# Performance work log

Measured on AMD Instinct MI355X. Metric: run time of the kernel, lower is better.

Reference implementation:

```python
import jax, jax.numpy as jnp
import numpy as np
from jax import lax

BN_EPS = 1e-3
SLOPE = 0.1
CLUSTER_TEMP = 30.0
K = 16
FEAT = 4096  # 8*8*64


def conv_bn_lrelu(x, w, b, g, beta, m, v):
    # Conv2d stride 2, padding 1 (NCHW / OIHW), then eval-mode BatchNorm, then LeakyReLU.
    y = lax.conv_general_dilated(x, w, window_strides=(2, 2), padding=((1, 1), (1, 1)),
                                 dimension_numbers=("NCHW", "OIHW", "NCHW"))
    y = y + b[None, :, None, None]
    scale = g / jnp.sqrt(v + BN_EPS)
    y = y * scale[None, :, None, None] + (beta - m * scale)[None, :, None, None]
    return jnp.where(y > 0, y, SLOPE * y)


def soft_kmeans(data, mu, num_iter, ct):
    # Row L2-normalize (equivalent to diag(1/||x||) @ data)
    data = data / jnp.linalg.norm(data, axis=1, keepdims=True)
    for _ in range(num_iter):
        dist = data @ mu.T                      # [N, K]
        r = jax.nn.softmax(ct * dist, axis=1)   # [N, K]
        mu = (r.T @ data) / r.sum(axis=0)[:, None]  # [K, F]
    dist = data @ mu.T
    r = jax.nn.softmax(ct * dist, axis=1)
    return mu, r, dist


def setup_inputs() -> dict:
    key = jax.random.key(0)
    ks = jax.random.split(key, 12)
    d = {}
    d["x"] = jax.random.normal(ks[0], (256, 3, 64, 64), dtype=jnp.float32)
    # conv1: 3 -> 128
    d["conv1_w"] = jax.random.normal(ks[1], (128, 3, 3, 3), dtype=jnp.float32) * 0.05
    d["conv1_b"] = jnp.zeros((128,), jnp.float32)
    d["bn1_g"] = jnp.ones((128,), jnp.float32)
    d["bn1_b"] = jnp.zeros((128,), jnp.float32)
    d["bn1_m"] = jax.random.normal(ks[2], (128,), dtype=jnp.float32) * 0.1
    d["bn1_v"] = jax.random.uniform(ks[3], (128,), minval=0.5, maxval=1.5, dtype=jnp.float32)
    # conv2: 128 -> 256
    d["conv2_w"] = jax.random.normal(ks[4], (256, 128, 3, 3), dtype=jnp.float32) * 0.02
    d["conv2_b"] = jnp.zeros((256,), jnp.float32)
    d["bn2_g"] = jnp.ones((256,), jnp.float32)
    d["bn2_b"] = jnp.zeros((256,), jnp.float32)
    d["bn2_m"] = jax.random.normal(ks[5], (256,), dtype=jnp.float32) * 0.1
    d["bn2_v"] = jax.random.uniform(ks[6], (256,), minval=0.5, maxval=1.5, dtype=jnp.float32)
    # conv3: 256 -> 64
    d["conv3_w"] = jax.random.normal(ks[7], (64, 256, 3, 3), dtype=jnp.float32) * 0.02
    d["conv3_b"] = jnp.zeros((64,), jnp.float32)
    d["bn3_g"] = jnp.ones((64,), jnp.float32)
    d["bn3_b"] = jnp.zeros((64,), jnp.float32)
    d["bn3_m"] = jax.random.normal(ks[8], (64,), dtype=jnp.float32) * 0.1
    d["bn3_v"] = jax.random.uniform(ks[9], (64,), minval=0.5, maxval=1.5, dtype=jnp.float32)
    # initial cluster centers, torch.rand(K, F)
    d["mu0"] = jax.random.uniform(ks[10], (K, FEAT), dtype=jnp.float32)
    d["num_iter"] = 10
    return d


def reference(x, conv1_w, conv1_b, bn1_g, bn1_b, bn1_m, bn1_v,
              conv2_w, conv2_b, bn2_g, bn2_b, bn2_m, bn2_v,
              conv3_w, conv3_b, bn3_g, bn3_b, bn3_m, bn3_v,
              mu0, num_iter):
    h = conv_bn_lrelu(x, conv1_w, conv1_b, bn1_g, bn1_b, bn1_m, bn1_v)   # [B,128,32,32]
    h = conv_bn_lrelu(h, conv2_w, conv2_b, bn2_g, bn2_b, bn2_m, bn2_v)   # [B,256,16,16]
    h = conv_bn_lrelu(h, conv3_w, conv3_b, bn3_g, bn3_b, bn3_m, bn3_v)   # [B,64,8,8]
    embeds = h.reshape(-1, FEAT)                                          # [B, 4096]
    mu_init, _, _ = soft_kmeans(embeds, mu0, num_iter, CLUSTER_TEMP)
    _, r, _ = soft_kmeans(embeds, lax.stop_gradient(mu_init), 1, CLUSTER_TEMP)
    return r
```

## Files before the change

kernel.cpp:

```cpp
#include <hip/hip_runtime.h>
#include <stdint.h>
#include <stddef.h>

typedef unsigned short u16;
typedef __attribute__((ext_vector_type(8))) short short8;
typedef __attribute__((ext_vector_type(4))) float f32x4;
typedef __attribute__((ext_vector_type(4))) int int4v;

__device__ __forceinline__ float bf2f(u16 u) {
    unsigned x = ((unsigned)u) << 16;
    return __uint_as_float(x);
}
__device__ __forceinline__ u16 f2bf(float f) {
    unsigned x = __float_as_uint(f);
    unsigned r = (x + 0x7fffu + ((x >> 16) & 1u)) >> 16;
    return (u16)r;
}
__device__ __forceinline__ float ldin(const void* p, size_t i, int isbf) {
    return isbf ? bf2f(((const u16*)p)[i]) : ((const float*)p)[i];
}
__device__ __forceinline__ int detect_bf(const void* v1) {
    const u16* ub = (const u16*)v1;
    int ok = 1;
#pragma unroll
    for (int i = 0; i < 16; i++) {
        float f = bf2f(ub[i]);
        if (!(f >= 0.4f && f <= 1.6f)) ok = 0;
    }
    return ok;
}
__device__ __forceinline__ int sw(int r, int c8) {
    return r * 32 + (((c8) ^ (r & 3)) << 3);
}

struct PrepArgs {
    const void *w1, *w2, *w3;
    u16 *W1p, *W2p, *W3p;
    const void *b1, *g1, *be1, *m1, *v1;
    const void *b2, *g2, *be2, *m2, *v2;
    const void *b3, *g3, *be3, *m3, *v3;
    float *es1, *esh1, *es2, *esh2, *es3, *esh3;
    u16 *zb;
};
__device__ __forceinline__ void packw_body(const void* src, u16* dst, int CI, int Kp,
                                           int total, int blk, int t, int isbf) {
    int p = blk * 256 + t;
    if (p >= total) return;
    int co = p / Kp, k = p - co * Kp;
    int tap = k / CI, ci = k - tap * CI;
    u16 v = 0;
    if (tap < 9) {
        size_t si = (size_t)(co * CI + ci) * 9 + tap;
        v = isbf ? ((const u16*)src)[si] : f2bf(((const float*)src)[si]);
    }
    dst[p] = v;
}
__global__ __launch_bounds__(256) void kprep_all(PrepArgs A) {
    int b = blockIdx.x, t = threadIdx.x;
    int isbf = detect_bf(A.v1);
    if (b < 1152) {
        packw_body(A.w2, A.W2p, 128, 1152, 256 * 1152, b, t, isbf);
    } else if (b < 1728) {
        packw_body(A.w3, A.W3p, 256, 2304, 64 * 2304, b - 1152, t, isbf);
    } else if (b < 1744) {
        packw_body(A.w1, A.W1p, 3, 32, 128 * 32, b - 1728, t, isbf);
    } else {
        if (b == 1745) A.zb[t] = 0;
        int u = (b - 1744) * 256 + t;
        const void *bb, *g, *be, *m, *v;
        float *es, *esh;
        int c;
        if (u < 128)      { c = u;       bb=A.b1; g=A.g1; be=A.be1; m=A.m1; v=A.v1; es=A.es1; esh=A.esh1; }
        else if (u < 384) { c = u - 128; bb=A.b2; g=A.g2; be=A.be2; m=A.m2; v=A.v2; es=A.es2; esh=A.esh2; }
        else if (u < 448) { c = u - 384; bb=A.b3; g=A.g3; be=A.be3; m=A.m3; v=A.v3; es=A.es3; esh=A.esh3; }
        else return;
        float sc = ldin(g, c, isbf) / sqrtf(ldin(v, c, isbf) + 1e-3f);
        float sh = (ldin(bb, c, isbf) - ldin(m, c, isbf)) * sc + ldin(be, c, isbf);
        es[c] = sc;
        esh[c] = sh;
    }
}

__global__ void kfallback(u16* __restrict__ out) {
    int i = blockIdx.x * 256 + threadIdx.x;
    if (i < 4096) out[i] = f2bf(0.0625f);
}

__global__ __launch_bounds__(256) void im2col1(const void* __restrict__ x,
                                               u16* __restrict__ A1,
                                               const void* __restrict__ v1ref) {
    int n = blockIdx.x, t = threadIdx.x;
    int isbf = detect_bf(v1ref);
    __shared__ u16 xs[3 * 64 * 64];
    if (isbf) {
        const u16* xp = (const u16*)x + (size_t)n * 12288;
#pragma unroll
        for (int i = t * 8; i < 12288; i += 2048)
            *(int4v*)&xs[i] = *(const int4v*)&xp[i];
    } else {
        const float* xp = (const float*)x + (size_t)n * 12288;
#pragma unroll
        for (int i = t * 4; i < 12288; i += 1024) {
            float4 v = *(const float4*)&xp[i];
            xs[i] = f2bf(v.x); xs[i + 1] = f2bf(v.y);
            xs[i + 2] = f2bf(v.z); xs[i + 3] = f2bf(v.w);
        }
    }
    __syncthreads();
#pragma unroll
    for (int rr = 0; rr < 4; rr++) {
        int m = rr * 256 + t;
        int ox = m & 31, oy = m >> 5;
        alignas(16) u16 row[32];
#pragma unroll
        for (int k = 0; k < 32; k++) {
            u16 val = 0;
            if (k < 27) {
                int tap = k / 3, ci = k - 3 * tap;
                int ky = tap / 3, kx = tap - 3 * ky;
                int iy = 2 * oy - 1 + ky, ix = 2 * ox - 1 + kx;
                if ((unsigned)iy < 64u && (unsigned)ix < 64u)
                    val = xs[ci * 4096 + iy * 64 + ix];
            }
            row[k] = val;
        }
        int4v* dst = (int4v*)(A1 + ((size_t)n * 1024 + m) * 32);
        const int4v* srcv = (const int4v*)row;
#pragma unroll
        for (int q = 0; q < 4; q++) dst[q] = srcv[q];
    }
}

__global__ __launch_bounds__(256) void gemm_conv1(
    const u16* __restrict__ A1, const u16* __restrict__ W,
    const float* __restrict__ es, const float* __restrict__ esh,
    u16* __restrict__ OutB) {
    alignas(16) __shared__ u16 As[128 * 32];
    alignas(16) __shared__ u16 Bs[128 * 32];
    const int t = threadIdx.x;
    const int m0 = blockIdx.x * 128;
    const int lane = t & 63, w = t >> 6;
    const int wm = w & 1, wn = w >> 1;
    const int rA = t >> 2, c8 = t & 3, koff = c8 * 8;

#pragma unroll
    for (int j = 0; j < 2; j++) {
        int4v va = *(const int4v*)(A1 + (size_t)(m0 + j * 64 + rA) * 32 + koff);
        *(int4v*)&As[sw(j * 64 + rA, c8)] = va;
        int4v vb = *(const int4v*)(W + (size_t)(j * 64 + rA) * 32 + koff);
        *(int4v*)&Bs[sw(j * 64 + rA, c8)] = vb;
    }
    __syncthreads();
    const int qc = lane >> 4, fr = lane & 15;
    short8 af[4], bf[4];
#pragma unroll
    for (int i = 0; i < 4; i++) af[i] = *(const short8*)&As[sw(wm * 64 + i * 16 + fr, qc)];
#pragma unroll
    for (int j = 0; j < 4; j++) bf[j] = *(const short8*)&Bs[sw(wn * 64 + j * 16 + fr, qc)];
    f32x4 acc[4][4];
#pragma unroll
    for (int i = 0; i < 4; i++)
#pragma unroll
        for (int j = 0; j < 4; j++) {
#pragma unroll
            for (int q = 0; q < 4; q++) acc[i][j][q] = 0.f;
            acc[i][j] = __builtin_amdgcn_mfma_f32_16x16x32_bf16(af[i], bf[j], acc[i][j], 0, 0, 0);
        }
    float scv[4], shv[4];
#pragma unroll
    for (int j = 0; j < 4; j++) {
        int c = wn * 64 + j * 16 + fr;
        scv[j] = es[c];
        shv[j] = esh[c];
    }
#pragma unroll
    for (int i = 0; i < 4; i++) {
#pragma unroll
        for (int rg = 0; rg < 4; rg++) {
            int m = m0 + wm * 64 + i * 16 + qc * 4 + rg;
            int ox = m & 31, oy = (m >> 5) & 31, n = m >> 10;
            u16* orow = OutB + ((size_t)(n * 32 + oy) * 32 + ox) * 128 + wn * 64 + fr;
#pragma unroll
            for (int j = 0; j < 4; j++) {
                float v = acc[i][j][rg] * scv[j] + shv[j];
                v = (v > 0.f) ? v : 0.1f * v;
                orow[j * 16] = f2bf(v);
            }
        }
    }
}

__global__ __launch_bounds__(512, 2) void gemm_conv2(
    const u16* __restrict__ h1, const u16* __restrict__ W,
    const float* __restrict__ es, const float* __restrict__ esh,
    u16* __restrict__ OutB, const u16* __restrict__ zb) {
    alignas(16) __shared__ u16 smem[4 * 16384];
    u16* const Ab0 = smem;
    u16* const Ab1 = smem + 16384;
    u16* const Bb0 = smem + 32768;
    u16* const Bb1 = smem + 49152;

    const int t = threadIdx.x;
    const int w = t >> 6, l = t & 63;
    const int img = blockIdx.x;
    const int wm = w >> 2, wn = w & 3;
    const int fr = l & 15, qc = l >> 4;

    int aiy0[4], aix0[4], ac8e[4];
    int brow[4];
#pragma unroll
    for (int i = 0; i < 4; ++i) {
        int gi = w * 256 + i * 64 + l;
        int r = gi >> 3, c8d = gi & 7;
        int c8s = c8d ^ (r & 7);
        int oy = r >> 4, ox = r & 15;
        aiy0[i] = 2 * oy - 1;
        aix0[i] = 2 * ox - 1;
        ac8e[i] = c8s * 8;
        brow[i] = r * 1152 + c8s * 8;
    }
    auto mkA = [&](int i, int ky, int kx) -> const u16* {
        int iy = aiy0[i] + ky, ix = aix0[i] + kx;
        if ((unsigned)iy < 32u && (unsigned)ix < 32u)
            return h1 + (size_t)(((img * 32 + iy) * 32 + ix) * 128 + ac8e[i]);
        return zb;
    };
    auto stage = [&](const u16* src, u16* ldsbase, int i) {
        __builtin_amdgcn_global_load_lds(
            (const __attribute__((address_space(1))) void*)src,
            (__attribute__((address_space(3))) void*)(ldsbase + (w * 4 + i) * 512),
            16, 0, 0);
    };

    f32x4 acc[8][4];
#pragma unroll
    for (int mi = 0; mi < 8; ++mi)
#pragma unroll
        for (int nj = 0; nj < 4; ++nj)
#pragma unroll
            for (int q = 0; q < 4; ++q) acc[mi][nj][q] = 0.0f;

    auto do_tile = [&](const u16* A, const u16* B) {
#pragma unroll
        for (int kk = 0; kk < 2; ++kk) {
            const int c8 = kk * 4 + qc;
            short8 a[8], b[4];
#pragma unroll
            for (int q = 0; q < 8; ++q) {
                int row = wm * 128 + q * 16 + fr;
                a[q] = *(const short8*)(A + row * 64 + ((c8 ^ (row & 7)) << 3));
            }
#pragma unroll
            for (int j = 0; j < 4; ++j) {
                int row = wn * 64 + j * 16 + fr;
                b[j] = *(const short8*)(B + row * 64 + ((c8 ^ (row & 7)) << 3));
            }
            __builtin_amdgcn_s_setprio(1);
#pragma unroll
            for (int q = 0; q < 8; ++q)
#pragma unroll
                for (int j = 0; j < 4; ++j)
                    acc[q][j] = __builtin_amdgcn_mfma_f32_16x16x32_bf16(
                        a[q], b[j], acc[q][j], 0, 0, 0);
            __builtin_amdgcn_s_setprio(0);
        }
    };

    const u16* pcur[4];
#pragma unroll
    for (int i = 0; i < 4; ++i) pcur[i] = mkA(i, 0, 0);
#pragma unroll
    for (int i = 0; i < 4; ++i) {
        stage(pcur[i], Ab0, i);
        stage(W + brow[i], Bb0, i);
    }

    for (int tap = 0; tap < 9; ++tap) {
        __syncthreads();
#pragma unroll
        for (int i = 0; i < 4; ++i) {
            stage(pcur[i] + 64, Ab1, i);
            stage(W + brow[i] + (2 * tap + 1) * 64, Bb1, i);
        }
        do_tile(Ab0, Bb0);
        __syncthreads();
        if (tap < 8) {
            const int tap2 = tap + 1;
            const int ky2 = (tap2 >= 6) ? 2 : (tap2 >= 3) ? 1 : 0;
            const int kx2 = tap2 - 3 * ky2;
#pragma unroll
            for (int i = 0; i < 4; ++i) pcur[i] = mkA(i, ky2, kx2);
#pragma unroll
            for (int i = 0; i < 4; ++i) {
                stage(pcur[i], Ab0, i);
                stage(W + brow[i] + (2 * tap + 2) * 64, Bb0, i);
            }
        }
        do_tile(Ab1, Bb1);
    }

    float scv[4], shv[4];
#pragma unroll
    for (int nj = 0; nj < 4; ++nj) {
        int c = wn * 64 + nj * 16 + fr;
        scv[nj] = es[c];
        shv[nj] = esh[c];
    }
#pragma unroll
    for (int mi = 0; mi < 8; ++mi) {
#pragma unroll
        for (int rg = 0; rg < 4; ++rg) {
            int r = wm * 128 + mi * 16 + qc * 4 + rg;
            u16* orow = OutB + ((size_t)img * 256 + r) * 256 + wn * 64 + fr;
#pragma unroll
            for (int nj = 0; nj < 4; ++nj) {
                float v = acc[mi][nj][rg] * scv[nj] + shv[nj];
                v = (v > 0.f) ? v : 0.1f * v;
                orow[nj * 16] = f2bf(v);
            }
        }
    }
}

__global__ __launch_bounds__(256) void gemm_conv3f(
    const u16* __restrict__ Asrc, const u16* __restrict__ W,
    const float* __restrict__ es3, const float* __restrict__ esh3,
    float* __restrict__ dat, u16* __restrict__ datbf) {
    constexpr int CIN = 256, KTOT = 2304, IH = 16;
    constexpr int CC = 8, SM = 2, SN = 2;

    alignas(16) __shared__ u16 As[64 * 32];
    alignas(16) __shared__ u16 Bs[64 * 32];
    __shared__ float red[4];

    const int t = threadIdx.x;
    const int lid = blockIdx.x;
    const int xcd = lid & 7, slot = lid >> 3;
    const int img = xcd * 32 + slot;
    const int m0 = img * 64;
    const int lane = t & 63, w = t >> 6;
    const int wm = w & 1, wn = w >> 1;
    const int rA = t >> 2, c8 = t & 3, koff = c8 * 8;
    const int fr = lane & 15, qc = lane >> 4;

    f32x4 acc[SM][SN];
#pragma unroll
    for (int i = 0; i < SM; i++)
#pragma unroll
        for (int j = 0; j < SN; j++)
#pragma unroll
            for (int q = 0; q < 4; q++) acc[i][j][q] = 0.0f;

    const int aox = rA & 7, aoy = (rA >> 3) & 7;
    auto mkoffs = [&](int tap) -> int {
        int ky = tap / 3, kx = tap - 3 * ky;
        int iy = 2 * aoy - 1 + ky, ix = 2 * aox - 1 + kx;
        if ((unsigned)iy < (unsigned)IH && (unsigned)ix < (unsigned)IH)
            return ((img * IH + iy) * IH + ix) * CIN;
        return -0x40000000;
    };
    const u16* Wrow = W + (size_t)rA * KTOT + koff;

    int offs_cur = mkoffs(0), offs_nxt;
    const int4v zerov = (int4v){0, 0, 0, 0};
    int4v bufA[2], bufB[2];
#pragma unroll
    for (int pp = 0; pp < 2; pp++) {
        bufA[pp] = (offs_cur >= 0)
                       ? *(const int4v*)(Asrc + offs_cur + pp * 32 + koff)
                       : zerov;
        bufB[pp] = *(const int4v*)(Wrow + pp * 32);
    }

    int flat = 0;
    for (int tap = 0; tap < 9; tap++) {
        offs_nxt = (tap < 8) ? mkoffs(tap + 1) : -0x40000000;
#pragma unroll
        for (int cc = 0; cc < CC; cc++, flat++) {
            const int pb_ = flat & 1;
            *(int4v*)&As[sw(rA, c8)] = bufA[pb_];
            *(int4v*)&Bs[sw(rA, c8)] = bufB[pb_];
            __syncthreads();
            {
                const int cc2 = cc + 2;
                const bool intap = (cc2 < CC);
                const int cci = intap ? cc2 : cc2 - CC;
                int o = intap ? offs_cur : offs_nxt;
                bufA[pb_] = (o >= 0) ? *(const int4v*)(Asrc + o + cci * 32 + koff) : zerov;
                const bool wvalid = intap || (tap < 8);
                const int wk = (intap ? tap : tap + 1) * CIN + cci * 32;
                bufB[pb_] = wvalid ? *(const int4v*)(Wrow + wk) : zerov;
            }
            short8 af[SM], bf[SN];
#pragma unroll
            for (int i = 0; i < SM; i++)
                af[i] = *(const short8*)&As[sw(wm * 32 + i * 16 + fr, qc)];
#pragma unroll
            for (int j = 0; j < SN; j++)
                bf[j] = *(const short8*)&Bs[sw(wn * 32 + j * 16 + fr, qc)];
#pragma unroll
            for (int i = 0; i < SM; i++)
#pragma unroll
                for (int j = 0; j < SN; j++)
                    acc[i][j] = __builtin_amdgcn_mfma_f32_16x16x32_bf16(
                        af[i], bf[j], acc[i][j], 0, 0, 0);
            __syncthreads();
        }
        offs_cur = offs_nxt;
    }

    float vals[SM][SN][4];
    float ssq = 0.f;
#pragma unroll
    for (int j = 0; j < SN; j++) {
        int c = wn * 32 + j * 16 + fr;
        float sc = es3[c], sh = esh3[c];
#pragma unroll
        for (int i = 0; i < SM; i++) {
#pragma unroll
            for (int rg = 0; rg < 4; rg++) {
                float v = acc[i][j][rg] * sc + sh;
                v = (v > 0.f) ? v : 0.1f * v;
                vals[i][j][rg] = v;
                ssq += v * v;
            }
        }
    }
#pragma unroll
    for (int off = 32; off > 0; off >>= 1) ssq += __shfl_xor(ssq, off);
    if (lane == 0) red[w] = ssq;
    __syncthreads();
    float inv = 1.0f / sqrtf(red[0] + red[1] + red[2] + red[3]);
#pragma unroll
    for (int j = 0; j < SN; j++) {
        int c = wn * 32 + j * 16 + fr;
#pragma unroll
        for (int i = 0; i < SM; i++) {
#pragma unroll
            for (int rg = 0; rg < 4; rg++) {
                int row = wm * 32 + i * 16 + qc * 4 + rg;
                size_t idx = (size_t)img * 4096 + c * 64 + row;
                float v = vals[i][j][rg] * inv;
                dat[idx] = v;
                datbf[idx] = f2bf(v);
            }
        }
    }
}

__global__ __launch_bounds__(256) void kgr(const u16* __restrict__ dbf,
                                           const float* __restrict__ dat,
                                           const void* __restrict__ mu0,
                                           float* __restrict__ Gp,
                                           float* __restrict__ rb0,
                                           const void* __restrict__ v1ref) {
    const int b = blockIdx.x, t = threadIdx.x;
    __shared__ float part[16][4];
    __shared__ float ds[16];

    if (b < 64) {
        const int tile = b & 15, s = b >> 4;
        const int m0 = (tile & 3) * 64, n0 = (tile >> 2) * 64;
        const int lane = t & 63, w = t >> 6;
        const int wm = w & 1, wn = w >> 1;
        const int fr = lane & 15, qc = lane >> 4;

        f32x4 acc[2][2];
#pragma unroll
        for (int i = 0; i < 2; i++)
#pragma unroll
            for (int j = 0; j < 2; j++)
#pragma unroll
                for (int q = 0; q < 4; q++) acc[i][j][q] = 0.0f;

        const u16* a0p = dbf + (size_t)(m0 + wm * 32 + fr) * 4096 + s * 1024 + qc * 8;
        const u16* a1p = a0p + 16 * 4096;
        const u16* b0p = dbf + (size_t)(n0 + wn * 32 + fr) * 4096 + s * 1024 + qc * 8;
        const u16* b1p = b0p + 16 * 4096;

        short8 Pa0[4], Pa1[4], Pb0[4], Pb1[4];
        short8 Qa0[4], Qa1[4], Qb0[4], Qb1[4];
        auto ldc = [&](short8* A0, short8* A1, short8* B0, short8* B1, int c) {
#pragma unroll
            for (int u = 0; u < 4; ++u) {
                const int o = c * 128 + u * 32;
                A0[u] = *(const short8*)(a0p + o);
                A1[u] = *(const short8*)(a1p + o);
                B0[u] = *(const short8*)(b0p + o);
                B1[u] = *(const short8*)(b1p + o);
            }
        };
        auto mmc = [&](short8* A0, short8* A1, short8* B0, short8* B1) {
#pragma unroll
            for (int u = 0; u < 4; ++u) {
                acc[0][0] = __builtin_amdgcn_mfma_f32_16x16x32_bf16(A0[u], B0[u], acc[0][0], 0, 0, 0);
                acc[0][1] = __builtin_amdgcn_mfma_f32_16x16x32_bf16(A0[u], B1[u], acc[0][1], 0, 0, 0);
                acc[1][0] = __builtin_amdgcn_mfma_f32_16x16x32_bf16(A1[u], B0[u], acc[1][0], 0, 0, 0);
                acc[1][1] = __builtin_amdgcn_mfma_f32_16x16x32_bf16(A1[u], B1[u], acc[1][1], 0, 0, 0);
            }
        };
        ldc(Pa0, Pa1, Pb0, Pb1, 0);
#pragma unroll
        for (int c = 0; c < 4; ++c) {
            ldc(Qa0, Qa1, Qb0, Qb1, 2 * c + 1);
            mmc(Pa0, Pa1, Pb0, Pb1);
            if (c < 3) ldc(Pa0, Pa1, Pb0, Pb1, 2 * c + 2);
            mmc(Qa0, Qa1, Qb0, Qb1);
        }

        float* gp = Gp + (size_t)s * 65536;
#pragma unroll
        for (int j = 0; j < 2; j++) {
            int cc = n0 + wn * 32 + j * 16 + fr;
#pragma unroll
            for (int i = 0; i < 2; i++)
#pragma unroll
                for (int rg = 0; rg < 4; rg++) {
                    int row = m0 + wm * 32 + i * 16 + qc * 4 + rg;
                    gp[row * 256 + cc] = acc[i][j][rg];
                }
        }
    } else {
        const int n = b - 64;
        const int isbf = detect_bf(v1ref);
        const int lane = t & 63, wv = t >> 6;
        float d[16];
#pragma unroll
        for (int j = 0; j < 16; j++) d[j] = dat[(size_t)n * 4096 + j * 256 + t];
#pragma unroll
        for (int k = 0; k < 16; k++) {
            float a = 0.f;
            if (isbf) {
                const u16* mp = (const u16*)mu0 + (size_t)k * 4096;
#pragma unroll
                for (int j = 0; j < 16; j++) a = fmaf(d[j], bf2f(mp[j * 256 + t]), a);
            } else {
                const float* mp = (const float*)mu0 + (size_t)k * 4096;
#pragma unroll
                for (int j = 0; j < 16; j++) a = fmaf(d[j], mp[j * 256 + t], a);
            }
#pragma unroll
            for (int off = 32; off > 0; off >>= 1) a += __shfl_xor(a, off);
            if (lane == 0) part[k][wv] = a;
        }
        __syncthreads();
        if (t < 16) {
            float dk = part[t][0] + part[t][1] + part[t][2] + part[t][3];
            ds[t] = dk;
            __syncthreads();
            float mx = -1e30f;
#pragma unroll
            for (int j = 0; j < 16; j++) mx = fmaxf(mx, ds[j]);
            float sum = 0.f;
#pragma unroll
            for (int j = 0; j < 16; j++) sum += __expf(30.f * (ds[j] - mx));
            rb0[n * 16 + t] = __expf(30.f * (dk - mx)) / sum;
        }
    }
}

__global__ __launch_bounds__(256) void kcomb(const float* __restrict__ Gp,
                                             u16* __restrict__ Ghi,
                                             u16* __restrict__ Glo) {
    const int i = (blockIdx.x * 256 + threadIdx.x) * 4;
    f32x4 s0 = *(const f32x4*)(Gp + i);
    f32x4 s1 = *(const f32x4*)(Gp + 65536 + i);
    f32x4 s2 = *(const f32x4*)(Gp + 131072 + i);
    f32x4 s3 = *(const f32x4*)(Gp + 196608 + i);
    unsigned long long ph = 0, pl = 0;
#pragma unroll
    for (int q = 0; q < 4; q++) {
        float v = ((s0[q] + s1[q]) + s2[q]) + s3[q];
        u16 hi = f2bf(v);
        u16 lo = f2bf(v - bf2f(hi));
        ph |= ((unsigned long long)hi) << (16 * q);
        pl |= ((unsigned long long)lo) << (16 * q);
    }
    *(unsigned long long*)(Ghi + i) = ph;
    *(unsigned long long*)(Glo + i) = pl;
}

__global__ __launch_bounds__(1024) void kmiter(const u16* __restrict__ Ghi,
                                               const u16* __restrict__ Glo,
                                               const float* __restrict__ rb0,
                                               void* __restrict__ dout,
                                               const void* __restrict__ v1ref) {
    const int t = threadIdx.x;
    const int isbf = detect_bf(v1ref);
    const int lane = t & 63, w = t >> 6;
    const int i0 = w * 16;
    const int col = lane & 15;
    const int q = lane >> 4;

    __shared__ u16 rThi[16 * 264];
    __shared__ u16 rTlo[16 * 264];
    __shared__ float part[16][17];

    const u16* Ahirow = Ghi + (size_t)(i0 + col) * 256 + q * 8;
    const u16* Alorow = Glo + (size_t)(i0 + col) * 256 + q * 8;

    {
        float rv[4];
#pragma unroll
        for (int rg = 0; rg < 4; rg++) {
            int row = i0 + q * 4 + rg;
            float v = rb0[row * 16 + col];
            rv[rg] = v;
            u16 hi = f2bf(v);
            rThi[col * 264 + row] = hi;
            rTlo[col * 264 + row] = f2bf(v - bf2f(hi));
        }
        float s0 = rv[0] + rv[1] + rv[2] + rv[3];
        s0 += __shfl_xor(s0, 16);
        s0 += __shfl_xor(s0, 32);
        if (lane < 16) part[w][lane] = s0;
    }
    __syncthreads();
    float rsc = 0.f;
#pragma unroll
    for (int ww = 0; ww < 16; ww++) rsc += part[ww][col];

    for (int iter = 0; iter < 11; iter++) {
        f32x4 acc = {0.f, 0.f, 0.f, 0.f};
#pragma unroll
        for (int s = 0; s < 8; s++) {
            short8 ah = *(const short8*)(Ahirow + s * 32);
            short8 al = *(const short8*)(Alorow + s * 32);
            short8 bh = *(const short8*)&rThi[col * 264 + s * 32 + q * 8];
            short8 bl = *(const short8*)&rTlo[col * 264 + s * 32 + q * 8];
            acc = __builtin_amdgcn_mfma_f32_16x16x32_bf16(ah, bh, acc, 0, 0, 0);
            acc = __builtin_amdgcn_mfma_f32_16x16x32_bf16(al, bh, acc, 0, 0, 0);
            acc = __builtin_amdgcn_mfma_f32_16x16x32_bf16(ah, bl, acc, 0, 0, 0);
        }
        float nv[4];
#pragma unroll
        for (int rg = 0; rg < 4; rg++) {
            float dk = acc[rg] / rsc;
            float mx = dk;
#pragma unroll
            for (int o = 1; o < 16; o <<= 1) mx = fmaxf(mx, __shfl_xor(mx, o));
            float e = __expf(30.f * (dk - mx));
            float ssum = e;
#pragma unroll
            for (int o = 1; o < 16; o <<= 1) ssum += __shfl_xor(ssum, o);
            nv[rg] = e / ssum;
        }
        if (iter < 10) {
            __syncthreads();
#pragma unroll
            for (int rg = 0; rg < 4; rg++) {
                int row = i0 + q * 4 + rg;
                u16 hi = f2bf(nv[rg]);
                rThi[col * 264 + row] = hi;
                rTlo[col * 264 + row] = f2bf(nv[rg] - bf2f(hi));
            }
            float s0 = nv[0] + nv[1] + nv[2] + nv[3];
            s0 += __shfl_xor(s0, 16);
            s0 += __shfl_xor(s0, 32);
            if (lane < 16) part[w][lane] = s0;
            __syncthreads();
            rsc = 0.f;
#pragma unroll
            for (int ww = 0; ww < 16; ww++) rsc += part[ww][col];
        } else {
#pragma unroll
            for (int rg = 0; rg < 4; rg++) {
                int row = i0 + q * 4 + rg;
                if (isbf) ((u16*)dout)[row * 16 + col] = f2bf(nv[rg]);
                else ((float*)dout)[row * 16 + col] = nv[rg];
            }
        }
    }
}

extern "C" void kernel_launch(void* const* d_in, const int* in_sizes, int n_in,
                              void* d_out, int out_size, void* d_ws, size_t ws_size,
                              hipStream_t stream) {
    const void* x   = d_in[0];
    const void* w1  = d_in[1];
    const void* b1  = d_in[2];
    const void* g1  = d_in[3];
    const void* be1 = d_in[4];
    const void* m1  = d_in[5];
    const void* v1  = d_in[6];
    const void* w2  = d_in[7];
    const void* b2  = d_in[8];
    const void* g2  = d_in[9];
    const void* be2 = d_in[10];
    const void* m2  = d_in[11];
    const void* v2  = d_in[12];
    const void* w3  = d_in[13];
    const void* b3  = d_in[14];
    const void* g3  = d_in[15];
    const void* be3 = d_in[16];
    const void* m3  = d_in[17];
    const void* v3  = d_in[18];
    const void* mu0 = d_in[19];

    char* p = (char*)d_ws;
    size_t used = 0;
    auto alloc = [&](size_t bytes) -> char* {
        char* q = p;
        size_t rb = (bytes + 255) & ~(size_t)255;
        p += rb;
        used += rb;
        return q;
    };
    float* rb0 = (float*)alloc(4096 * 4);
    u16* Ghi = (u16*)alloc((size_t)65536 * 2);
    u16* Glo = (u16*)alloc((size_t)65536 * 2);
    float* Gp = (float*)alloc((size_t)4 * 65536 * 4);
    u16* W1p = (u16*)alloc((size_t)128 * 32 * 2);
    u16* W2p = (u16*)alloc((size_t)256 * 1152 * 2);
    u16* W3p = (u16*)alloc((size_t)64 * 2304 * 2);
    float* es1 = (float*)alloc(128 * 4);
    float* esh1 = (float*)alloc(128 * 4);
    float* es2 = (float*)alloc(256 * 4);
    float* esh2 = (float*)alloc(256 * 4);
    float* es3 = (float*)alloc(64 * 4);
    float* esh3 = (float*)alloc(64 * 4);
    u16* zb = (u16*)alloc(512);
    const size_t R1 = (size_t)256 * 32 * 32 * 128 * 2;
    const size_t R2 = (size_t)256 * 16 * 16 * 256 * 2;
    char* reg1 = alloc(R1);
    char* reg2 = alloc(R2);
    u16* h1 = (u16*)reg1;
    u16* A1 = (u16*)reg2;
    u16* h2 = (u16*)reg2;
    float* dat = (float*)reg1;
    u16* datbf = (u16*)(reg1 + 4194304);

    if (used > ws_size) {
        kfallback<<<16, 256, 0, stream>>>((u16*)d_out);
        return;
    }

    PrepArgs pa = {w1, w2, w3, W1p, W2p, W3p,
                   b1, g1, be1, m1, v1, b2, g2, be2, m2, v2, b3, g3, be3, m3, v3,
                   es1, esh1, es2, esh2, es3, esh3, zb};
    kprep_all<<<1746, 256, 0, stream>>>(pa);
    im2col1<<<256, 256, 0, stream>>>(x, A1, v1);
    gemm_conv1<<<dim3(2048), 256, 0, stream>>>(A1, W1p, es1, esh1, h1);
    gemm_conv2<<<dim3(256), 512, 0, stream>>>(h1, W2p, es2, esh2, h2, zb);
    gemm_conv3f<<<dim3(256), 256, 0, stream>>>(h2, W3p, es3, esh3, dat, datbf);
    kgr<<<dim3(320), 256, 0, stream>>>(datbf, dat, mu0, Gp, rb0, v1);
    kcomb<<<dim3(64), 256, 0, stream>>>(Gp, Ghi, Glo);
    kmiter<<<1, 1024, 0, stream>>>(Ghi, Glo, rb0, d_out, v1);
}
```

Before: 252.5 us.

## Pipeline conv2 staging with vmcnt waits and double-buffer kmeans LDS

The conv GEMM loop now issues the next buffer's global-to-LDS staging before computing the current one. It waits with partial vmcnt counts and raw s_barrier instead of full __syncthreads, so loads stay in flight across tiles. The k-means iteration kernel double-buffers its responsibility matrices and partial sums in LDS, removing one barrier per iteration. It also splits the MFMA accumulation into two independent chains to shorten dependency stalls. The hand-tuned vmcnt counts are fragile and depend on exactly how many memory ops each stage issues.

```diff
diff --git a/kernel.cpp b/kernel.cpp
--- a/kernel.cpp
+++ b/kernel.cpp
@@ -274,16 +274,18 @@
         stage(pcur[i], Ab0, i);
         stage(W + brow[i], Bb0, i);
     }
+#pragma unroll
+    for (int i = 0; i < 4; ++i) {
+        stage(pcur[i] + 64, Ab1, i);
+        stage(W + brow[i] + 64, Bb1, i);
+    }
 
     for (int tap = 0; tap < 9; ++tap) {
-        __syncthreads();
-#pragma unroll
-        for (int i = 0; i < 4; ++i) {
-            stage(pcur[i] + 64, Ab1, i);
-            stage(W + brow[i] + (2 * tap + 1) * 64, Bb1, i);
-        }
+        asm volatile("s_waitcnt vmcnt(8)" ::: "memory");
+        __builtin_amdgcn_s_barrier();
         do_tile(Ab0, Bb0);
-        __syncthreads();
+        asm volatile("s_waitcnt lgkmcnt(0)" ::: "memory");
+        __builtin_amdgcn_s_barrier();
         if (tap < 8) {
             const int tap2 = tap + 1;
             const int ky2 = (tap2 >= 6) ? 2 : (tap2 >= 3) ? 1 : 0;
@@ -296,7 +298,22 @@
                 stage(W + brow[i] + (2 * tap + 2) * 64, Bb0, i);
             }
         }
+        if (tap < 8) {
+            asm volatile("s_waitcnt vmcnt(8)" ::: "memory");
+        } else {
+            asm volatile("s_waitcnt vmcnt(0)" ::: "memory");
+        }
+        __builtin_amdgcn_s_barrier();
         do_tile(Ab1, Bb1);
+        asm volatile("s_waitcnt lgkmcnt(0)" ::: "memory");
+        __builtin_amdgcn_s_barrier();
+        if (tap < 8) {
+#pragma unroll
+            for (int i = 0; i < 4; ++i) {
+                stage(pcur[i] + 64, Ab1, i);
+                stage(W + brow[i] + (2 * tap + 3) * 64, Bb1, i);
+            }
+        }
     }
 
     float scv[4], shv[4];
@@ -592,9 +609,9 @@
     const int col = lane & 15;
     const int q = lane >> 4;
 
-    __shared__ u16 rThi[16 * 264];
-    __shared__ u16 rTlo[16 * 264];
-    __shared__ float part[16][17];
+    __shared__ u16 rThi[2][16 * 264];
+    __shared__ u16 rTlo[2][16 * 264];
+    __shared__ float part[2][16][17];
 
     const u16* Ahirow = Ghi + (size_t)(i0 + col) * 256 + q * 8;
     const u16* Alorow = Glo + (size_t)(i0 + col) * 256 + q * 8;
@@ -607,35 +624,48 @@
             float v = rb0[row * 16 + col];
             rv[rg] = v;
             u16 hi = f2bf(v);
-            rThi[col * 264 + row] = hi;
-            rTlo[col * 264 + row] = f2bf(v - bf2f(hi));
+            rThi[0][col * 264 + row] = hi;
+            rTlo[0][col * 264 + row] = f2bf(v - bf2f(hi));
         }
         float s0 = rv[0] + rv[1] + rv[2] + rv[3];
         s0 += __shfl_xor(s0, 16);
         s0 += __shfl_xor(s0, 32);
-        if (lane < 16) part[w][lane] = s0;
+        if (lane < 16) part[0][w][lane] = s0;
     }
     __syncthreads();
     float rsc = 0.f;
 #pragma unroll
-    for (int ww = 0; ww < 16; ww++) rsc += part[ww][col];
-
+    for (int ww = 0; ww < 16; ww++) rsc += part[0][ww][col];
+
+    int cur = 0;
     for (int iter = 0; iter < 11; iter++) {
-        f32x4 acc = {0.f, 0.f, 0.f, 0.f};
-#pragma unroll
-        for (int s = 0; s < 8; s++) {
-            short8 ah = *(const short8*)(Ahirow + s * 32);
-            short8 al = *(const short8*)(Alorow + s * 32);
-            short8 bh = *(const short8*)&rThi[col * 264 + s * 32 + q * 8];
-            short8 bl = *(const short8*)&rTlo[col * 264 + s * 32 + q * 8];
-            acc = __builtin_amdgcn_mfma_f32_16x16x32_bf16(ah, bh, acc, 0, 0, 0);
-            acc = __builtin_amdgcn_mfma_f32_16x16x32_bf16(al, bh, acc, 0, 0, 0);
-            acc = __builtin_amdgcn_mfma_f32_16x16x32_bf16(ah, bl, acc, 0, 0, 0);
+        f32x4 acc0 = {0.f, 0.f, 0.f, 0.f};
+        f32x4 acc1 = {0.f, 0.f, 0.f, 0.f};
+#pragma unroll
+        for (int s = 0; s < 4; s++) {
+            {
+                short8 ah = *(const short8*)(Ahirow + s * 32);
+                short8 al = *(const short8*)(Alorow + s * 32);
+                short8 bh = *(const short8*)&rThi[cur][col * 264 + s * 32 + q * 8];
+                short8 bl = *(const short8*)&rTlo[cur][col * 264 + s * 32 + q * 8];
+                acc0 = __builtin_amdgcn_mfma_f32_16x16x32_bf16(ah, bh, acc0, 0, 0, 0);
+                acc0 = __builtin_amdgcn_mfma_f32_16x16x32_bf16(al, bh, acc0, 0, 0, 0);
+                acc0 = __builtin_amdgcn_mfma_f32_16x16x32_bf16(ah, bl, acc0, 0, 0, 0);
+            }
+            {
+                short8 ah = *(const short8*)(Ahirow + (s + 4) * 32);
+                short8 al = *(const short8*)(Alorow + (s + 4) * 32);
+                short8 bh = *(const short8*)&rThi[cur][col * 264 + (s + 4) * 32 + q * 8];
+                short8 bl = *(const short8*)&rTlo[cur][col * 264 + (s + 4) * 32 + q * 8];
+                acc1 = __builtin_amdgcn_mfma_f32_16x16x32_bf16(ah, bh, acc1, 0, 0, 0);
+                acc1 = __builtin_amdgcn_mfma_f32_16x16x32_bf16(al, bh, acc1, 0, 0, 0);
+                acc1 = __builtin_amdgcn_mfma_f32_16x16x32_bf16(ah, bl, acc1, 0, 0, 0);
+            }
         }
         float nv[4];
 #pragma unroll
         for (int rg = 0; rg < 4; rg++) {
-            float dk = acc[rg] / rsc;
+            float dk = (acc0[rg] + acc1[rg]) / rsc;
             float mx = dk;
 #pragma unroll
             for (int o = 1; o < 16; o <<= 1) mx = fmaxf(mx, __shfl_xor(mx, o));
@@ -646,22 +676,23 @@
             nv[rg] = e / ssum;
         }
         if (iter < 10) {
-            __syncthreads();
+            const int nxt = cur ^ 1;
 #pragma unroll
             for (int rg = 0; rg < 4; rg++) {
                 int row = i0 + q * 4 + rg;
                 u16 hi = f2bf(nv[rg]);
-                rThi[col * 264 + row] = hi;
-                rTlo[col * 264 + row] = f2bf(nv[rg] - bf2f(hi));
+                rThi[nxt][col * 264 + row] = hi;
+                rTlo[nxt][col * 264 + row] = f2bf(nv[rg] - bf2f(hi));
             }
             float s0 = nv[0] + nv[1] + nv[2] + nv[3];
             s0 += __shfl_xor(s0, 16);
             s0 += __shfl_xor(s0, 32);
-            if (lane < 16) part[w][lane] = s0;
+            if (lane < 16) part[nxt][w][lane] = s0;
             __syncthreads();
             rsc = 0.f;
 #pragma unroll
-            for (int ww = 0; ww < 16; ww++) rsc += part[ww][col];
+            for (int ww = 0; ww < 16; ww++) rsc += part[nxt][ww][col];
+            cur = nxt;
         } else {
 #pragma unroll
             for (int rg = 0; rg < 4; rg++) {
```

Measured after the change: 268.5 us. 6.3% more time.
